# Kernel tuning notes

Hardware: AMD Instinct MI355X
Metric: run time of the kernel (lower is better)

The kernel has to match this reference:

```python
import jax, jax.numpy as jnp
import numpy as np

EPS = 1e-5

def _pw1d(W, b, x):  # W (O,C), x (B,C,N) -> (B,O,N); 1x1 Conv1d
    return jnp.einsum('oc,bcn->bon', W, x) + b[None, :, None]

def _pw2d(W, b, x):  # W (O,C), x (B,C,N,K) -> (B,O,N,K); 1x1 Conv2d
    return jnp.einsum('oc,bcnk->bonk', W, x) + b[None, :, None, None]

def _bn(x, g, b, m, v):  # BatchNorm2d, eval mode, over channel axis 1
    scale = g / jnp.sqrt(v + EPS)
    return (x - m[None, :, None, None]) * scale[None, :, None, None] + b[None, :, None, None]

def _knn(pos, k):  # pos (B,3,N) -> idx (B,N,K) of nearest neighbors (incl. self)
    p = jnp.transpose(pos, (0, 2, 1))             # (B,N,3)
    sq = jnp.sum(p * p, axis=-1)                  # (B,N)
    d = sq[:, :, None] - 2.0 * jnp.einsum('bid,bjd->bij', p, p) + sq[:, None, :]
    _, idx = jax.lax.top_k(-d, k)
    return idx

def _gather(feat, idx):  # feat (B,C,N), idx (B,N,K) -> (B,C,N,K)
    return jax.vmap(lambda f, i: f[:, i])(feat, idx)


def setup_inputs() -> dict:
    key = jax.random.key(0)
    B, C, N, H, AH, K = 4, 64, 4096, 64, 256, 16
    ks = jax.random.split(key, 32)
    s = lambda i, shp, sc=0.05: jax.random.normal(ks[i], shp, dtype=jnp.float32) * sc
    u = lambda i, shp: jax.random.uniform(ks[i], shp, dtype=jnp.float32, minval=0.5, maxval=1.5)
    return {
        'x': jax.random.normal(ks[0], (B, 3, N), dtype=jnp.float32),
        'y': jax.random.normal(ks[1], (B, C, N), dtype=jnp.float32),
        'W_start': s(2, (C, C)), 'b_start': s(3, (C,)),
        'W_key': s(4, (C, C)), 'b_key': s(5, (C,)),
        'W_query': s(6, (C, 3)), 'b_query': s(7, (C,)),
        'P1': s(8, (H, 3)), 'pb1': s(9, (H,)),
        'bn1_g': u(10, (H,)), 'bn1_b': s(11, (H,)), 'bn1_m': s(12, (H,)), 'bn1_v': u(13, (H,)),
        'P2': s(14, (C, H)), 'pb2': s(15, (C,)),
        'A1': s(16, (AH, C)), 'ab1': s(17, (AH,)),
        'bn2_g': u(18, (AH,)), 'bn2_b': s(19, (AH,)), 'bn2_m': s(20, (AH,)), 'bn2_v': u(21, (AH,)),
        'A2': s(22, (C, AH)), 'ab2': s(23, (C,)),
        'W_end': s(24, (C, C)), 'b_end': s(25, (C,)),
        'n_knn': 16,
    }


def reference(x, y, W_start, b_start, W_key, b_key, W_query, b_query,
              P1, pb1, bn1_g, bn1_b, bn1_m, bn1_v, P2, pb2,
              A1, ab1, bn2_g, bn2_b, bn2_m, bn2_v, A2, ab2,
              W_end, b_end, n_knn):
    identity = y
    y1 = _pw1d(W_start, b_start, y)                 # linear_start, (B,C,N)
    idx = _knn(x, n_knn)                            # (B,N,K)
    key = _pw1d(W_key, b_key, y1)
    value = y1
    query = _pw1d(W_query, b_query, x)              # 3 -> C pointwise
    key_g = _gather(key, idx)                       # (B,C,N,K)
    qk_rel = query[..., None] - key_g
    pos_rel = x[..., None] - _gather(x, idx)        # (B,3,N,K)
    pe = _pw2d(P2, pb2, jax.nn.relu(_bn(_pw2d(P1, pb1, pos_rel), bn1_g, bn1_b, bn1_m, bn1_v)))
    attn = _pw2d(A2, ab2, jax.nn.relu(_bn(_pw2d(A1, ab1, qk_rel + pe), bn2_g, bn2_b, bn2_m, bn2_v)))
    attn = jax.nn.softmax(attn, axis=-1)            # softmax over neighbor axis
    val = value[..., None] + pe                     # (B,C,N,K)
    agg = jnp.sum(attn * val, axis=-1)              # einsum 'bcij,bcij->bci'
    out = _pw1d(W_end, b_end, agg) + identity
    return out
```

## Files before the change

kernel.cpp:

```cpp
#include <hip/hip_runtime.h>
#include <hip/hip_bf16.h>

#define BB 4
#define CC 64
#define NN 4096
#define HH 64
#define AH 256
#define KNN 16
#define EPSV 1e-5f
#define PREP_NB 32

typedef __attribute__((ext_vector_type(8))) short short8;
typedef __attribute__((ext_vector_type(4))) short short4v;
typedef __attribute__((ext_vector_type(4))) unsigned short ushort4v;
typedef __attribute__((ext_vector_type(4))) float floatx4;

__device__ __forceinline__ unsigned short f2bf(float f) {
    unsigned u = __float_as_uint(f);
    u += 0x7FFFu + ((u >> 16) & 1u);
    return (unsigned short)(u >> 16);
}
__device__ __forceinline__ float bf2f(unsigned short u) {
    return __uint_as_float(((unsigned)u) << 16);
}

__device__ __forceinline__ unsigned long long umin64(unsigned long long a, unsigned long long b) {
    return a < b ? a : b;
}
__device__ __forceinline__ unsigned long long umax64(unsigned long long a, unsigned long long b) {
    return a > b ? a : b;
}
__device__ __forceinline__ unsigned long long shfl_xor_u64(unsigned long long v, int m) {
    int lo = __shfl_xor((int)(unsigned)(v & 0xFFFFFFFFull), m);
    int hi = __shfl_xor((int)(unsigned)(v >> 32), m);
    return ((unsigned long long)(unsigned)hi << 32) | (unsigned)lo;
}

__global__ void prep_params(const float* __restrict__ P1, const float* __restrict__ pb1,
                            const float* __restrict__ P2, const float* __restrict__ A1,
                            const float* __restrict__ ab1, const float* __restrict__ A2,
                            const float* __restrict__ g1, const float* __restrict__ b1,
                            const float* __restrict__ m1, const float* __restrict__ v1,
                            const float* __restrict__ g2, const float* __restrict__ b2,
                            const float* __restrict__ m2, const float* __restrict__ v2,
                            const float* __restrict__ Wend, const float* __restrict__ Ws,
                            const float* __restrict__ Wk, const float* __restrict__ Wq,
                            const float* __restrict__ bq,
                            unsigned short* __restrict__ A1L, unsigned short* __restrict__ A2L,
                            unsigned short* __restrict__ P2L, unsigned short* __restrict__ WendL,
                            unsigned short* __restrict__ WsL, unsigned short* __restrict__ WkL,
                            float* __restrict__ Wq4, float* __restrict__ P1p,
                            float* __restrict__ ab1f, float* __restrict__ bn2s_c) {
    int t0 = threadIdx.x;
    int t = blockIdx.x * 256 + t0;
    const int stride = PREP_NB * 256;
    if (blockIdx.x == 0) {
        if (t0 < HH) {
            float s = g1[t0] * rsqrtf(v1[t0] + EPSV);
            float c = b1[t0] - m1[t0] * s;
            P1p[4 * t0 + 0] = P1[3 * t0 + 0] * s;
            P1p[4 * t0 + 1] = P1[3 * t0 + 1] * s;
            P1p[4 * t0 + 2] = P1[3 * t0 + 2] * s;
            P1p[4 * t0 + 3] = pb1[t0] * s + c;
        }
        if (t0 < AH) {
            float s = g2[t0] * rsqrtf(v2[t0] + EPSV);
            bn2s_c[t0] = s;
            ab1f[t0] = ab1[t0] * s + (b2[t0] - m2[t0] * s);
        }
        if (t0 < CC) {
            Wq4[4 * t0 + 0] = Wq[3 * t0 + 0];
            Wq4[4 * t0 + 1] = Wq[3 * t0 + 1];
            Wq4[4 * t0 + 2] = Wq[3 * t0 + 2];
            Wq4[4 * t0 + 3] = bq[t0];
        }
    }
    for (int i = t; i < 16384; i += stride) {
        int e = i & 7, lane = (i >> 3) & 63, ks = (i >> 9) & 1, ht = i >> 10;
        int m = lane & 15, q = lane >> 4;
        A1L[i] = f2bf(A1[(ht * 16 + m) * CC + ks * 32 + q * 8 + e]);
    }
    for (int i = t; i < 16384; i += stride) {
        int e = i & 7, lane = (i >> 3) & 63, kk = (i >> 9) & 7, nt = i >> 12;
        int m = lane & 15, q = lane >> 4;
        A2L[i] = f2bf(A2[(nt * 16 + m) * AH + kk * 32 + q * 8 + e]);
    }
    for (int i = t; i < 4096; i += stride) {
        int e = i & 7, lane = (i >> 3) & 63, ks = (i >> 9) & 1, nt = i >> 10;
        int m = lane & 15, q = lane >> 4;
        P2L[i] = f2bf(P2[(nt * 16 + m) * HH + ks * 32 + q * 8 + e]);
    }
    for (int i = t; i < 4096; i += stride) {
        int e = i & 7, lane = (i >> 3) & 63, ks = (i >> 9) & 1, wv = i >> 10;
        int m = lane & 15, q = lane >> 4;
        WendL[i] = f2bf(Wend[(wv * 16 + m) * CC + ks * 32 + q * 8 + e]);
    }
    for (int i = t; i < 8192; i += stride) {
        int e = i & 7, lane = (i >> 3) & 63, ks = (i >> 9) & 1, ot = i >> 10;
        int m = lane & 15, q = lane >> 4;
        WsL[i] = f2bf(Ws[(ot * 16 + m) * CC + ks * 32 + q * 8 + e]);
    }
    for (int i = t; i < 8192; i += stride) {
        int e = i & 7, lane = (i >> 3) & 63, ks = (i >> 9) & 1, ot = i >> 10;
        int m = lane & 15, q = lane >> 4;
        WkL[i] = f2bf(Wk[(ot * 16 + m) * CC + ks * 32 + q * 8 + e]);
    }
}

#define UPITCH 68
#define HPITCH 68

__device__ __forceinline__ short8 lds_frag(const unsigned short* p) {
    short4v lo = *(const short4v*)p;
    short4v hi = *(const short4v*)(p + 4);
    short8 v;
    v[0] = lo[0]; v[1] = lo[1]; v[2] = lo[2]; v[3] = lo[3];
    v[4] = hi[0]; v[5] = hi[1]; v[6] = hi[2]; v[7] = hi[3];
    return v;
}

__global__ __launch_bounds__(64) void prep_features(
    const float* __restrict__ x, const float* __restrict__ y,
    const unsigned short* __restrict__ WsL, const float* __restrict__ bs,
    const unsigned short* __restrict__ WkL, const float* __restrict__ bk,
    const float* __restrict__ Wq4,
    unsigned short* __restrict__ y1bf, unsigned short* __restrict__ keybf,
    unsigned short* __restrict__ qrybf) {
    __shared__ unsigned short t_lds[16 * UPITCH];

    int b = blockIdx.x >> 8;
    int n0 = (blockIdx.x & 255) << 4;
    int lane = threadIdx.x;
    int m = lane & 15, quad = lane >> 4;
    size_t ybase = (size_t)b * CC * NN;

    short8 yA[2];
#pragma unroll
    for (int ks = 0; ks < 2; ++ks)
#pragma unroll
        for (int j = 0; j < 8; ++j)
            yA[ks][j] = (short)f2bf(y[ybase + (size_t)(ks * 32 + quad * 8 + j) * NN + n0 + m]);

#pragma unroll
    for (int ot = 0; ot < 4; ++ot) {
        short8 b0 = *(const short8*)(WsL + ((ot * 2 + 0) * 64 + lane) * 8);
        short8 b1 = *(const short8*)(WsL + ((ot * 2 + 1) * 64 + lane) * 8);
        floatx4 acc = (floatx4){0.f, 0.f, 0.f, 0.f};
        acc = __builtin_amdgcn_mfma_f32_16x16x32_bf16(yA[0], b0, acc, 0, 0, 0);
        acc = __builtin_amdgcn_mfma_f32_16x16x32_bf16(yA[1], b1, acc, 0, 0, 0);
        float bsv = bs[ot * 16 + m];
#pragma unroll
        for (int r = 0; r < 4; ++r)
            t_lds[(4 * quad + r) * UPITCH + ot * 16 + m] = f2bf(acc[r] + bsv);
    }
    __syncthreads();

    short8 uA[2];
#pragma unroll
    for (int ks = 0; ks < 2; ++ks)
        uA[ks] = lds_frag(&t_lds[m * UPITCH + ks * 32 + quad * 8]);

    int p = lane >> 2, ck = lane & 3;
    size_t obase = ((size_t)b * NN + n0 + p) * CC + ck * 16;
#pragma unroll
    for (int s = 0; s < 4; ++s)
        *(ushort4v*)(y1bf + obase + s * 4) =
            *(const ushort4v*)&t_lds[p * UPITCH + ck * 16 + s * 4];
    __syncthreads();

#pragma unroll
    for (int ot = 0; ot < 4; ++ot) {
        short8 b0 = *(const short8*)(WkL + ((ot * 2 + 0) * 64 + lane) * 8);
        short8 b1 = *(const short8*)(WkL + ((ot * 2 + 1) * 64 + lane) * 8);
        floatx4 acc = (floatx4){0.f, 0.f, 0.f, 0.f};
        acc = __builtin_amdgcn_mfma_f32_16x16x32_bf16(uA[0], b0, acc, 0, 0, 0);
        acc = __builtin_amdgcn_mfma_f32_16x16x32_bf16(uA[1], b1, acc, 0, 0, 0);
        float bkv = bk[ot * 16 + m];
#pragma unroll
        for (int r = 0; r < 4; ++r)
            t_lds[(4 * quad + r) * UPITCH + ot * 16 + m] = f2bf(acc[r] + bkv);
    }
    __syncthreads();
#pragma unroll
    for (int s = 0; s < 4; ++s)
        *(ushort4v*)(keybf + obase + s * 4) =
            *(const ushort4v*)&t_lds[p * UPITCH + ck * 16 + s * 4];

    float x0 = x[(size_t)(b * 3 + 0) * NN + n0 + p];
    float x1 = x[(size_t)(b * 3 + 1) * NN + n0 + p];
    float x2 = x[(size_t)(b * 3 + 2) * NN + n0 + p];
#pragma unroll
    for (int s = 0; s < 4; ++s) {
        ushort4v pk;
#pragma unroll
        for (int e = 0; e < 4; ++e) {
            int ch = ck * 16 + s * 4 + e;
            const float4 w = *(const float4*)(Wq4 + 4 * ch);
            pk[e] = f2bf(w.x * x0 + w.y * x1 + w.z * x2 + w.w);
        }
        *(ushort4v*)(qrybf + obase + s * 4) = pk;
    }
}

__global__ __launch_bounds__(256) void knn_kernel(const float* __restrict__ x,
                                                  int* __restrict__ idx_out) {
    __shared__ __align__(16) char smem[65536];
    float4* pts = (float4*)smem;
    unsigned long long* surv = (unsigned long long*)smem;

    int b = blockIdx.x >> 10;
    int grp = blockIdx.x & 1023;
    int w = threadIdx.x >> 6;
    int lane = threadIdx.x & 63;
    int n = (grp << 2) + w;

    const float* xb = x + (size_t)b * 3 * NN;
    for (int i = threadIdx.x; i < NN; i += 256)
        pts[i] = make_float4(xb[i], xb[NN + i], xb[2 * NN + i], 0.f);
    __syncthreads();

    float4 q = pts[n];

    float dreg[64];
    float vmin = 3.4e38f;
#pragma unroll
    for (int r = 0; r < 64; ++r) {
        float4 c = pts[(r << 6) + lane];
        float ax = q.x - c.x, ay = q.y - c.y, az = q.z - c.z;
        float d = ax * ax + ay * ay + az * az;
        dreg[r] = d;
        vmin = fminf(vmin, d);
    }
#pragma unroll
    for (int k = 2; k <= 64; k <<= 1) {
#pragma unroll
        for (int j = k >> 1; j > 0; j >>= 1) {
            float o = __shfl_xor(vmin, j);
            bool lower = (lane & j) == 0;
            bool up = (lane & k) == 0;
            float mn = fminf(vmin, o), mx = fmaxf(vmin, o);
            vmin = (lower == up) ? mn : mx;
        }
    }
    float T = __shfl(vmin, 15);

    __syncthreads();

    unsigned long long* buf = surv + (w << 7);
    unsigned cnt = 0;
#pragma unroll
    for (int r = 0; r < 64; ++r) {
        float d = dreg[r];
        bool hit = d <= T;
        unsigned long long mask = __ballot(hit);
        if (hit) {
            unsigned off = cnt + (unsigned)__popcll(mask & ((1ull << lane) - 1ull));
            if (off < 128) {
                int j = (r << 6) + lane;
                buf[off] = ((unsigned long long)__float_as_uint(d) << 32) | (unsigned)j;
            }
        }
        cnt += (unsigned)__popcll(mask);
    }
    if (cnt > 128) cnt = 128;

    unsigned long long v0 = (lane < (int)cnt) ? buf[lane] : 0xFFFFFFFFFFFFFFFFull;
    unsigned long long v1 = (lane + 64 < (int)cnt) ? buf[lane + 64] : 0xFFFFFFFFFFFFFFFFull;
#pragma unroll
    for (int k = 2; k <= 128; k <<= 1) {
#pragma unroll
        for (int j = k >> 1; j > 0; j >>= 1) {
            if (j >= 64) {
                unsigned long long lo = umin64(v0, v1), hi = umax64(v0, v1);
                v0 = lo; v1 = hi;
            } else {
                bool lower = (lane & j) == 0;
                unsigned long long o0 = shfl_xor_u64(v0, j);
                bool up0 = ((lane & k) == 0);
                v0 = (lower == up0) ? umin64(v0, o0) : umax64(v0, o0);
                unsigned long long o1 = shfl_xor_u64(v1, j);
                bool up1 = (((64 + lane) & k) == 0);
                v1 = (lower == up1) ? umin64(v1, o1) : umax64(v1, o1);
            }
        }
    }
    if (lane < KNN)
        idx_out[((size_t)b * NN + n) * KNN + lane] = (int)(unsigned)(v0 & 0xFFFFFFFFull);
}

__global__ __launch_bounds__(256, 3) void attn_mfma(
    const float* __restrict__ x, const float* __restrict__ y,
    const unsigned short* __restrict__ y1bf, const unsigned short* __restrict__ keybf,
    const unsigned short* __restrict__ qrybf, const int* __restrict__ idx,
    const float* __restrict__ P1p, const unsigned short* __restrict__ P2L,
    const float* __restrict__ pb2, const unsigned short* __restrict__ A1L,
    const float* __restrict__ ab1f, const float* __restrict__ bn2s_c,
    const unsigned short* __restrict__ A2L, const unsigned short* __restrict__ WendL,
    const float* __restrict__ bend,
    float* __restrict__ out) {
    __shared__ unsigned short u_lds[128 * UPITCH];
    __shared__ unsigned short hid_lds[128 * HPITCH];
    __shared__ float agg_lds[8 * 68];
    __shared__ float outstage[512];

    int blk = blockIdx.x;
    int b = blk & 3;
    int n0 = (blk >> 2) << 3;
    int w = threadIdx.x >> 6;
    int lane = threadIdx.x & 63;
    int m = lane & 15, quad = lane >> 4;

    int pt[2];
    size_t bpt[2];
#pragma unroll
    for (int t = 0; t < 2; ++t) {
        pt[t] = n0 + 2 * w + t;
        bpt[t] = (size_t)b * NN + pt[t];
    }

    int jm[2], j4[2][4];
    unsigned short qu[2][4], kvu[2][4][4];
#pragma unroll
    for (int t = 0; t < 2; ++t) {
        jm[t] = idx[bpt[t] * KNN + m];
#pragma unroll
        for (int r = 0; r < 4; ++r) j4[t][r] = idx[bpt[t] * KNN + 4 * quad + r];
#pragma unroll
        for (int nt = 0; nt < 4; ++nt) {
            qu[t][nt] = qrybf[bpt[t] * CC + nt * 16 + m];
#pragma unroll
            for (int r = 0; r < 4; ++r)
                kvu[t][nt][r] = keybf[((size_t)b * NN + j4[t][r]) * CC + nt * 16 + m];
        }
    }

    short8 h1A[2][2];
#pragma unroll
    for (int t = 0; t < 2; ++t) {
        float dx = x[(size_t)(b * 3 + 0) * NN + pt[t]] - x[(size_t)(b * 3 + 0) * NN + jm[t]];
        float dy = x[(size_t)(b * 3 + 1) * NN + pt[t]] - x[(size_t)(b * 3 + 1) * NN + jm[t]];
        float dz = x[(size_t)(b * 3 + 2) * NN + pt[t]] - x[(size_t)(b * 3 + 2) * NN + jm[t]];
#pragma unroll
        for (int ks = 0; ks < 2; ++ks)
#pragma unroll
            for (int j = 0; j < 8; ++j) {
                int h1 = ks * 32 + quad * 8 + j;
                const float4 p = *(const float4*)(P1p + 4 * h1);
                float a = fmaxf(p.x * dx + p.y * dy + p.z * dz + p.w, 0.f);
                h1A[t][ks][j] = (short)f2bf(a);
            }
    }

    floatx4 pacc[2][4];
#pragma unroll
    for (int t = 0; t < 2; ++t)
#pragma unroll
        for (int nt = 0; nt < 4; ++nt) pacc[t][nt] = (floatx4){0.f, 0.f, 0.f, 0.f};
#pragma unroll
    for (int ks = 0; ks < 2; ++ks)
#pragma unroll
        for (int nt = 0; nt < 4; ++nt) {
            short8 bb = *(const short8*)(P2L + ((nt * 2 + ks) * 64 + lane) * 8);
            pacc[0][nt] = __builtin_amdgcn_mfma_f32_16x16x32_bf16(h1A[0][ks], bb, pacc[0][nt], 0, 0, 0);
            pacc[1][nt] = __builtin_amdgcn_mfma_f32_16x16x32_bf16(h1A[1][ks], bb, pacc[1][nt], 0, 0, 0);
        }
#pragma unroll
    for (int nt = 0; nt < 4; ++nt) {
        float pb = pb2[nt * 16 + m];
#pragma unroll
        for (int t = 0; t < 2; ++t)
#pragma unroll
            for (int r = 0; r < 4; ++r) pacc[t][nt][r] += pb;
    }

#pragma unroll
    for (int t = 0; t < 2; ++t)
#pragma unroll
        for (int nt = 0; nt < 4; ++nt) {
            float qv = bf2f(qu[t][nt]);
#pragma unroll
            for (int r = 0; r < 4; ++r) {
                float uu = qv - bf2f(kvu[t][nt][r]) + pacc[t][nt][r];
                u_lds[(w * 32 + t * 16 + 4 * quad + r) * UPITCH + nt * 16 + m] = f2bf(uu);
            }
        }

    short8 uA[2][2];
#pragma unroll
    for (int t = 0; t < 2; ++t)
#pragma unroll
        for (int ks = 0; ks < 2; ++ks)
            uA[t][ks] = lds_frag(&u_lds[(w * 32 + t * 16 + m) * UPITCH + ks * 32 + quad * 8]);

    floatx4 acc2[2][4];
#pragma unroll
    for (int t = 0; t < 2; ++t)
#pragma unroll
        for (int nt = 0; nt < 4; ++nt) acc2[t][nt] = (floatx4){0.f, 0.f, 0.f, 0.f};

    for (int qd = 0; qd < 4; ++qd) {
#pragma unroll
        for (int nt4 = 0; nt4 < 4; ++nt4) {
            int ht = qd * 4 + nt4;
            const unsigned short* a1t = A1L + ht * 1024 + lane * 8;
            short8 b0 = *(const short8*)(a1t);
            short8 b1 = *(const short8*)(a1t + 512);
            int h = ht * 16 + m;
            float s = bn2s_c[h], t0 = ab1f[h];
#pragma unroll
            for (int t = 0; t < 2; ++t) {
                floatx4 acc = (floatx4){0.f, 0.f, 0.f, 0.f};
                acc = __builtin_amdgcn_mfma_f32_16x16x32_bf16(uA[t][0], b0, acc, 0, 0, 0);
                acc = __builtin_amdgcn_mfma_f32_16x16x32_bf16(uA[t][1], b1, acc, 0, 0, 0);
#pragma unroll
                for (int r = 0; r < 4; ++r) {
                    float hv = fmaxf(acc[r] * s + t0, 0.f);
                    hid_lds[(w * 32 + t * 16 + 4 * quad + r) * HPITCH + nt4 * 16 + m] = f2bf(hv);
                }
            }
        }
        short8 hA[2][2];
#pragma unroll
        for (int t = 0; t < 2; ++t)
#pragma unroll
            for (int ks = 0; ks < 2; ++ks)
                hA[t][ks] = lds_frag(&hid_lds[(w * 32 + t * 16 + m) * HPITCH + ks * 32 + quad * 8]);
#pragma unroll
        for (int ks = 0; ks < 2; ++ks)
#pragma unroll
            for (int nt = 0; nt < 4; ++nt) {
                int kk = qd * 2 + ks;
                short8 bb = *(const short8*)(A2L + ((nt * 8 + kk) * 64 + lane) * 8);
                acc2[0][nt] = __builtin_amdgcn_mfma_f32_16x16x32_bf16(hA[0][ks], bb, acc2[0][nt], 0, 0, 0);
                acc2[1][nt] = __builtin_amdgcn_mfma_f32_16x16x32_bf16(hA[1][ks], bb, acc2[1][nt], 0, 0, 0);
            }
    }

#pragma unroll
    for (int t = 0; t < 2; ++t)
#pragma unroll
        for (int nt = 0; nt < 4; ++nt) {
            float l0 = acc2[t][nt][0], l1 = acc2[t][nt][1];
            float l2 = acc2[t][nt][2], l3 = acc2[t][nt][3];
            float mx = fmaxf(fmaxf(l0, l1), fmaxf(l2, l3));
            mx = fmaxf(mx, __shfl_xor(mx, 16));
            mx = fmaxf(mx, __shfl_xor(mx, 32));
            float e0 = __expf(l0 - mx), e1 = __expf(l1 - mx);
            float e2 = __expf(l2 - mx), e3 = __expf(l3 - mx);
            float sum = (e0 + e1) + (e2 + e3);
            sum += __shfl_xor(sum, 16);
            sum += __shfl_xor(sum, 32);
            float y1v = bf2f(y1bf[bpt[t] * CC + nt * 16 + m]);
            float contrib = e0 * (y1v + pacc[t][nt][0]) + e1 * (y1v + pacc[t][nt][1]) +
                            e2 * (y1v + pacc[t][nt][2]) + e3 * (y1v + pacc[t][nt][3]);
            contrib += __shfl_xor(contrib, 16);
            contrib += __shfl_xor(contrib, 32);
            float agg = contrib / sum;
            if (quad == 0) agg_lds[(2 * w + t) * 68 + nt * 16 + m] = agg;
        }
    __syncthreads();

    short8 aggA[2];
#pragma unroll
    for (int ks = 0; ks < 2; ++ks)
#pragma unroll
        for (int j = 0; j < 8; ++j)
            aggA[ks][j] = (short)f2bf(agg_lds[(m & 7) * 68 + ks * 32 + quad * 8 + j]);
    short8 wb0 = *(const short8*)(WendL + ((w * 2 + 0) * 64 + lane) * 8);
    short8 wb1 = *(const short8*)(WendL + ((w * 2 + 1) * 64 + lane) * 8);
    floatx4 facc = (floatx4){0.f, 0.f, 0.f, 0.f};
    facc = __builtin_amdgcn_mfma_f32_16x16x32_bf16(aggA[0], wb0, facc, 0, 0, 0);
    facc = __builtin_amdgcn_mfma_f32_16x16x32_bf16(aggA[1], wb1, facc, 0, 0, 0);
    if (quad < 2) {
        float be = bend[w * 16 + m];
#pragma unroll
        for (int r = 0; r < 4; ++r)
            outstage[(w * 16 + m) * 8 + 4 * quad + r] = facc[r] + be;
    }
    __syncthreads();

    int t2 = threadIdx.x;
    int o = t2 >> 2, pp = (t2 & 3) * 2;
#pragma unroll
    for (int e = 0; e < 2; ++e) {
        size_t oi = ((size_t)(b * CC + o)) * NN + n0 + pp + e;
        out[oi] = outstage[o * 8 + pp + e] + y[oi];
    }
}

extern "C" void kernel_launch(void* const* d_in, const int* in_sizes, int n_in,
                              void* d_out, int out_size, void* d_ws, size_t ws_size,
                              hipStream_t stream) {
    const float* x    = (const float*)d_in[0];
    const float* y    = (const float*)d_in[1];
    const float* Ws   = (const float*)d_in[2];
    const float* bs   = (const float*)d_in[3];
    const float* Wk   = (const float*)d_in[4];
    const float* bk   = (const float*)d_in[5];
    const float* Wq   = (const float*)d_in[6];
    const float* bq   = (const float*)d_in[7];
    const float* P1   = (const float*)d_in[8];
    const float* pb1  = (const float*)d_in[9];
    const float* g1   = (const float*)d_in[10];
    const float* b1   = (const float*)d_in[11];
    const float* m1   = (const float*)d_in[12];
    const float* v1   = (const float*)d_in[13];
    const float* P2   = (const float*)d_in[14];
    const float* pb2  = (const float*)d_in[15];
    const float* A1   = (const float*)d_in[16];
    const float* ab1  = (const float*)d_in[17];
    const float* g2   = (const float*)d_in[18];
    const float* b2   = (const float*)d_in[19];
    const float* m2   = (const float*)d_in[20];
    const float* v2   = (const float*)d_in[21];
    const float* A2   = (const float*)d_in[22];
    const float* ab2  = (const float*)d_in[23];
    const float* Wend = (const float*)d_in[24];
    const float* bend = (const float*)d_in[25];
    (void)ab2;

    unsigned short* usws = (unsigned short*)d_ws;
    unsigned short* y1bf  = usws;
    unsigned short* keybf = usws + 1048576;
    unsigned short* qrybf = usws + 2097152;
    int* idx = (int*)(usws + 3145728);
    unsigned short* A1L = usws + 3670016;
    unsigned short* A2L = A1L + 16384;
    unsigned short* P2L = A2L + 16384;
    unsigned short* WsL = P2L + 4096;
    unsigned short* WkL = WsL + 8192;
    unsigned short* WendL = WkL + 8192;
    float* Wq4   = (float*)(WendL + 4096);
    float* P1p   = Wq4 + 256;
    float* ab1f  = P1p + 256;
    float* bn2sc = ab1f + 256;
    float* out   = (float*)d_out;

    hipLaunchKernelGGL(prep_params, dim3(PREP_NB), dim3(256), 0, stream,
                       P1, pb1, P2, A1, ab1, A2, g1, b1, m1, v1, g2, b2, m2, v2,
                       Wend, Ws, Wk, Wq, bq,
                       A1L, A2L, P2L, WendL, WsL, WkL, Wq4, P1p, ab1f, bn2sc);
    hipLaunchKernelGGL(prep_features, dim3(1024), dim3(64), 0, stream,
                       x, y, WsL, bs, WkL, bk, Wq4, y1bf, keybf, qrybf);
    hipLaunchKernelGGL(knn_kernel, dim3(4096), dim3(256), 0, stream, x, idx);
    hipLaunchKernelGGL(attn_mfma, dim3(2048), dim3(256), 0, stream,
                       x, y, y1bf, keybf, qrybf, idx,
                       P1p, P2L, pb2, A1L, ab1f, bn2sc, A2L, WendL,
                       bend, out);
}
```

Before: 242.0 us.

## Fuse param prep, feature prep and kNN into one heterogeneous kernel

Merges the three pre-attention kernels into a single launch whose blocks branch by index into kNN, feature projection, or parameter-relayout roles. This removes two launches and their serialization. The kNN path now handles two query points per wave, and the distance uses an expanded form with precomputed squared norms plus a monotone float-to-uint key. Feature blocks convert the Ws/Wk weights to bf16 on the fly instead of reading a prelaid buffer. Risks include register pressure from two 64-entry distance arrays, the 64KB LDS footprint now applying to the feature and param blocks too, and small numeric differences from the expanded distance formula.

```diff
diff --git a/kernel.cpp b/kernel.cpp
--- a/kernel.cpp
+++ b/kernel.cpp
@@ -8,7 +8,10 @@
 #define AH 256
 #define KNN 16
 #define EPSV 1e-5f
-#define PREP_NB 32
+
+#define KNN_BLKS 2048
+#define PF_BLKS 256
+#define PP_BLKS 32
 
 typedef __attribute__((ext_vector_type(8))) short short8;
 typedef __attribute__((ext_vector_type(4))) short short4v;
@@ -23,7 +26,6 @@
 __device__ __forceinline__ float bf2f(unsigned short u) {
     return __uint_as_float(((unsigned)u) << 16);
 }
-
 __device__ __forceinline__ unsigned long long umin64(unsigned long long a, unsigned long long b) {
     return a < b ? a : b;
 }
@@ -35,76 +37,9 @@
     int hi = __shfl_xor((int)(unsigned)(v >> 32), m);
     return ((unsigned long long)(unsigned)hi << 32) | (unsigned)lo;
 }
-
-__global__ void prep_params(const float* __restrict__ P1, const float* __restrict__ pb1,
-                            const float* __restrict__ P2, const float* __restrict__ A1,
-                            const float* __restrict__ ab1, const float* __restrict__ A2,
-                            const float* __restrict__ g1, const float* __restrict__ b1,
-                            const float* __restrict__ m1, const float* __restrict__ v1,
-                            const float* __restrict__ g2, const float* __restrict__ b2,
-                            const float* __restrict__ m2, const float* __restrict__ v2,
-                            const float* __restrict__ Wend, const float* __restrict__ Ws,
-                            const float* __restrict__ Wk, const float* __restrict__ Wq,
-                            const float* __restrict__ bq,
-                            unsigned short* __restrict__ A1L, unsigned short* __restrict__ A2L,
-                            unsigned short* __restrict__ P2L, unsigned short* __restrict__ WendL,
-                            unsigned short* __restrict__ WsL, unsigned short* __restrict__ WkL,
-                            float* __restrict__ Wq4, float* __restrict__ P1p,
-                            float* __restrict__ ab1f, float* __restrict__ bn2s_c) {
-    int t0 = threadIdx.x;
-    int t = blockIdx.x * 256 + t0;
-    const int stride = PREP_NB * 256;
-    if (blockIdx.x == 0) {
-        if (t0 < HH) {
-            float s = g1[t0] * rsqrtf(v1[t0] + EPSV);
-            float c = b1[t0] - m1[t0] * s;
-            P1p[4 * t0 + 0] = P1[3 * t0 + 0] * s;
-            P1p[4 * t0 + 1] = P1[3 * t0 + 1] * s;
-            P1p[4 * t0 + 2] = P1[3 * t0 + 2] * s;
-            P1p[4 * t0 + 3] = pb1[t0] * s + c;
-        }
-        if (t0 < AH) {
-            float s = g2[t0] * rsqrtf(v2[t0] + EPSV);
-            bn2s_c[t0] = s;
-            ab1f[t0] = ab1[t0] * s + (b2[t0] - m2[t0] * s);
-        }
-        if (t0 < CC) {
-            Wq4[4 * t0 + 0] = Wq[3 * t0 + 0];
-            Wq4[4 * t0 + 1] = Wq[3 * t0 + 1];
-            Wq4[4 * t0 + 2] = Wq[3 * t0 + 2];
-            Wq4[4 * t0 + 3] = bq[t0];
-        }
-    }
-    for (int i = t; i < 16384; i += stride) {
-        int e = i & 7, lane = (i >> 3) & 63, ks = (i >> 9) & 1, ht = i >> 10;
-        int m = lane & 15, q = lane >> 4;
-        A1L[i] = f2bf(A1[(ht * 16 + m) * CC + ks * 32 + q * 8 + e]);
-    }
-    for (int i = t; i < 16384; i += stride) {
-        int e = i & 7, lane = (i >> 3) & 63, kk = (i >> 9) & 7, nt = i >> 12;
-        int m = lane & 15, q = lane >> 4;
-        A2L[i] = f2bf(A2[(nt * 16 + m) * AH + kk * 32 + q * 8 + e]);
-    }
-    for (int i = t; i < 4096; i += stride) {
-        int e = i & 7, lane = (i >> 3) & 63, ks = (i >> 9) & 1, nt = i >> 10;
-        int m = lane & 15, q = lane >> 4;
-        P2L[i] = f2bf(P2[(nt * 16 + m) * HH + ks * 32 + q * 8 + e]);
-    }
-    for (int i = t; i < 4096; i += stride) {
-        int e = i & 7, lane = (i >> 3) & 63, ks = (i >> 9) & 1, wv = i >> 10;
-        int m = lane & 15, q = lane >> 4;
-        WendL[i] = f2bf(Wend[(wv * 16 + m) * CC + ks * 32 + q * 8 + e]);
-    }
-    for (int i = t; i < 8192; i += stride) {
-        int e = i & 7, lane = (i >> 3) & 63, ks = (i >> 9) & 1, ot = i >> 10;
-        int m = lane & 15, q = lane >> 4;
-        WsL[i] = f2bf(Ws[(ot * 16 + m) * CC + ks * 32 + q * 8 + e]);
-    }
-    for (int i = t; i < 8192; i += stride) {
-        int e = i & 7, lane = (i >> 3) & 63, ks = (i >> 9) & 1, ot = i >> 10;
-        int m = lane & 15, q = lane >> 4;
-        WkL[i] = f2bf(Wk[(ot * 16 + m) * CC + ks * 32 + q * 8 + e]);
-    }
+__device__ __forceinline__ unsigned fmono(float d) {
+    unsigned u = __float_as_uint(d);
+    return ((int)u < 0) ? ~u : (u | 0x80000000u);
 }
 
 #define UPITCH 68
@@ -119,173 +54,261 @@
     return v;
 }
 
-__global__ __launch_bounds__(64) void prep_features(
+__global__ __launch_bounds__(256) void fused_prep_knn(
     const float* __restrict__ x, const float* __restrict__ y,
-    const unsigned short* __restrict__ WsL, const float* __restrict__ bs,
-    const unsigned short* __restrict__ WkL, const float* __restrict__ bk,
-    const float* __restrict__ Wq4,
+    const float* __restrict__ Ws, const float* __restrict__ bs,
+    const float* __restrict__ Wk, const float* __restrict__ bk,
+    const float* __restrict__ Wq, const float* __restrict__ bq,
+    const float* __restrict__ P1, const float* __restrict__ pb1,
+    const float* __restrict__ P2, const float* __restrict__ A1,
+    const float* __restrict__ ab1, const float* __restrict__ A2,
+    const float* __restrict__ g1, const float* __restrict__ b1v,
+    const float* __restrict__ m1, const float* __restrict__ v1,
+    const float* __restrict__ g2, const float* __restrict__ b2v,
+    const float* __restrict__ m2, const float* __restrict__ v2,
+    const float* __restrict__ Wend,
+    int* __restrict__ idx_out,
     unsigned short* __restrict__ y1bf, unsigned short* __restrict__ keybf,
-    unsigned short* __restrict__ qrybf) {
-    __shared__ unsigned short t_lds[16 * UPITCH];
-
-    int b = blockIdx.x >> 8;
-    int n0 = (blockIdx.x & 255) << 4;
-    int lane = threadIdx.x;
-    int m = lane & 15, quad = lane >> 4;
-    size_t ybase = (size_t)b * CC * NN;
-
-    short8 yA[2];
-#pragma unroll
-    for (int ks = 0; ks < 2; ++ks)
-#pragma unroll
-        for (int j = 0; j < 8; ++j)
-            yA[ks][j] = (short)f2bf(y[ybase + (size_t)(ks * 32 + quad * 8 + j) * NN + n0 + m]);
-
-#pragma unroll
-    for (int ot = 0; ot < 4; ++ot) {
-        short8 b0 = *(const short8*)(WsL + ((ot * 2 + 0) * 64 + lane) * 8);
-        short8 b1 = *(const short8*)(WsL + ((ot * 2 + 1) * 64 + lane) * 8);
-        floatx4 acc = (floatx4){0.f, 0.f, 0.f, 0.f};
-        acc = __builtin_amdgcn_mfma_f32_16x16x32_bf16(yA[0], b0, acc, 0, 0, 0);
-        acc = __builtin_amdgcn_mfma_f32_16x16x32_bf16(yA[1], b1, acc, 0, 0, 0);
-        float bsv = bs[ot * 16 + m];
-#pragma unroll
-        for (int r = 0; r < 4; ++r)
-            t_lds[(4 * quad + r) * UPITCH + ot * 16 + m] = f2bf(acc[r] + bsv);
-    }
-    __syncthreads();
-
-    short8 uA[2];
-#pragma unroll
-    for (int ks = 0; ks < 2; ++ks)
-        uA[ks] = lds_frag(&t_lds[m * UPITCH + ks * 32 + quad * 8]);
-
-    int p = lane >> 2, ck = lane & 3;
-    size_t obase = ((size_t)b * NN + n0 + p) * CC + ck * 16;
-#pragma unroll
-    for (int s = 0; s < 4; ++s)
-        *(ushort4v*)(y1bf + obase + s * 4) =
-            *(const ushort4v*)&t_lds[p * UPITCH + ck * 16 + s * 4];
-    __syncthreads();
-
-#pragma unroll
-    for (int ot = 0; ot < 4; ++ot) {
-        short8 b0 = *(const short8*)(WkL + ((ot * 2 + 0) * 64 + lane) * 8);
-        short8 b1 = *(const short8*)(WkL + ((ot * 2 + 1) * 64 + lane) * 8);
-        floatx4 acc = (floatx4){0.f, 0.f, 0.f, 0.f};
-        acc = __builtin_amdgcn_mfma_f32_16x16x32_bf16(uA[0], b0, acc, 0, 0, 0);
-        acc = __builtin_amdgcn_mfma_f32_16x16x32_bf16(uA[1], b1, acc, 0, 0, 0);
-        float bkv = bk[ot * 16 + m];
-#pragma unroll
-        for (int r = 0; r < 4; ++r)
-            t_lds[(4 * quad + r) * UPITCH + ot * 16 + m] = f2bf(acc[r] + bkv);
-    }
-    __syncthreads();
-#pragma unroll
-    for (int s = 0; s < 4; ++s)
-        *(ushort4v*)(keybf + obase + s * 4) =
-            *(const ushort4v*)&t_lds[p * UPITCH + ck * 16 + s * 4];
-
-    float x0 = x[(size_t)(b * 3 + 0) * NN + n0 + p];
-    float x1 = x[(size_t)(b * 3 + 1) * NN + n0 + p];
-    float x2 = x[(size_t)(b * 3 + 2) * NN + n0 + p];
-#pragma unroll
-    for (int s = 0; s < 4; ++s) {
-        ushort4v pk;
-#pragma unroll
-        for (int e = 0; e < 4; ++e) {
-            int ch = ck * 16 + s * 4 + e;
-            const float4 w = *(const float4*)(Wq4 + 4 * ch);
-            pk[e] = f2bf(w.x * x0 + w.y * x1 + w.z * x2 + w.w);
-        }
-        *(ushort4v*)(qrybf + obase + s * 4) = pk;
-    }
-}
-
-__global__ __launch_bounds__(256) void knn_kernel(const float* __restrict__ x,
-                                                  int* __restrict__ idx_out) {
+    unsigned short* __restrict__ qrybf,
+    unsigned short* __restrict__ A1L, unsigned short* __restrict__ A2L,
+    unsigned short* __restrict__ P2L, unsigned short* __restrict__ WendL,
+    float* __restrict__ P1p, float* __restrict__ ab1f, float* __restrict__ bn2s_c) {
     __shared__ __align__(16) char smem[65536];
-    float4* pts = (float4*)smem;
-    unsigned long long* surv = (unsigned long long*)smem;
-
-    int b = blockIdx.x >> 10;
-    int grp = blockIdx.x & 1023;
+    int blk = blockIdx.x;
+    int lane = threadIdx.x & 63;
     int w = threadIdx.x >> 6;
-    int lane = threadIdx.x & 63;
-    int n = (grp << 2) + w;
-
-    const float* xb = x + (size_t)b * 3 * NN;
-    for (int i = threadIdx.x; i < NN; i += 256)
-        pts[i] = make_float4(xb[i], xb[NN + i], xb[2 * NN + i], 0.f);
-    __syncthreads();
-
-    float4 q = pts[n];
-
-    float dreg[64];
-    float vmin = 3.4e38f;
-#pragma unroll
-    for (int r = 0; r < 64; ++r) {
-        float4 c = pts[(r << 6) + lane];
-        float ax = q.x - c.x, ay = q.y - c.y, az = q.z - c.z;
-        float d = ax * ax + ay * ay + az * az;
-        dreg[r] = d;
-        vmin = fminf(vmin, d);
-    }
-#pragma unroll
-    for (int k = 2; k <= 64; k <<= 1) {
-#pragma unroll
-        for (int j = k >> 1; j > 0; j >>= 1) {
-            float o = __shfl_xor(vmin, j);
-            bool lower = (lane & j) == 0;
-            bool up = (lane & k) == 0;
-            float mn = fminf(vmin, o), mx = fmaxf(vmin, o);
-            vmin = (lower == up) ? mn : mx;
-        }
-    }
-    float T = __shfl(vmin, 15);
-
-    __syncthreads();
-
-    unsigned long long* buf = surv + (w << 7);
-    unsigned cnt = 0;
-#pragma unroll
-    for (int r = 0; r < 64; ++r) {
-        float d = dreg[r];
-        bool hit = d <= T;
-        unsigned long long mask = __ballot(hit);
-        if (hit) {
-            unsigned off = cnt + (unsigned)__popcll(mask & ((1ull << lane) - 1ull));
-            if (off < 128) {
-                int j = (r << 6) + lane;
-                buf[off] = ((unsigned long long)__float_as_uint(d) << 32) | (unsigned)j;
-            }
-        }
-        cnt += (unsigned)__popcll(mask);
-    }
-    if (cnt > 128) cnt = 128;
-
-    unsigned long long v0 = (lane < (int)cnt) ? buf[lane] : 0xFFFFFFFFFFFFFFFFull;
-    unsigned long long v1 = (lane + 64 < (int)cnt) ? buf[lane + 64] : 0xFFFFFFFFFFFFFFFFull;
-#pragma unroll
-    for (int k = 2; k <= 128; k <<= 1) {
-#pragma unroll
-        for (int j = k >> 1; j > 0; j >>= 1) {
-            if (j >= 64) {
-                unsigned long long lo = umin64(v0, v1), hi = umax64(v0, v1);
-                v0 = lo; v1 = hi;
-            } else {
-                bool lower = (lane & j) == 0;
-                unsigned long long o0 = shfl_xor_u64(v0, j);
-                bool up0 = ((lane & k) == 0);
-                v0 = (lower == up0) ? umin64(v0, o0) : umax64(v0, o0);
-                unsigned long long o1 = shfl_xor_u64(v1, j);
-                bool up1 = (((64 + lane) & k) == 0);
-                v1 = (lower == up1) ? umin64(v1, o1) : umax64(v1, o1);
-            }
-        }
-    }
-    if (lane < KNN)
-        idx_out[((size_t)b * NN + n) * KNN + lane] = (int)(unsigned)(v0 & 0xFFFFFFFFull);
+
+    if (blk < KNN_BLKS) {
+        float4* pts = (float4*)smem;
+        unsigned long long* surv = (unsigned long long*)smem;
+
+        int b = blk >> 9;
+        int grp = blk & 511;
+        const float* xb = x + (size_t)b * 3 * NN;
+        for (int i = threadIdx.x; i < NN; i += 256) {
+            float cx = xb[i], cy = xb[NN + i], cz = xb[2 * NN + i];
+            pts[i] = make_float4(cx, cy, cz, cx * cx + cy * cy + cz * cz);
+        }
+        __syncthreads();
+
+        int n0 = (grp << 3) + (w << 1);
+        float4 q0 = pts[n0], q1 = pts[n0 + 1];
+        float q0x = -2.f * q0.x, q0y = -2.f * q0.y, q0z = -2.f * q0.z, q0w = q0.w;
+        float q1x = -2.f * q1.x, q1y = -2.f * q1.y, q1z = -2.f * q1.z, q1w = q1.w;
+
+        float d0reg[64], d1reg[64];
+        float vmin0 = 3.4e38f, vmin1 = 3.4e38f;
+#pragma unroll
+        for (int r = 0; r < 64; ++r) {
+            float4 c = pts[(r << 6) + lane];
+            float d0 = fmaf(q0x, c.x, fmaf(q0y, c.y, fmaf(q0z, c.z, c.w + q0w)));
+            float d1 = fmaf(q1x, c.x, fmaf(q1y, c.y, fmaf(q1z, c.z, c.w + q1w)));
+            d0reg[r] = d0; d1reg[r] = d1;
+            vmin0 = fminf(vmin0, d0);
+            vmin1 = fminf(vmin1, d1);
+        }
+
+        float T[2];
+#pragma unroll
+        for (int t = 0; t < 2; ++t) {
+            float v = t ? vmin1 : vmin0;
+#pragma unroll
+            for (int k = 2; k <= 64; k <<= 1) {
+#pragma unroll
+                for (int j = k >> 1; j > 0; j >>= 1) {
+                    float o = __shfl_xor(v, j);
+                    bool lower = (lane & j) == 0;
+                    bool up = (lane & k) == 0;
+                    float mn = fminf(v, o), mx = fmaxf(v, o);
+                    v = (lower == up) ? mn : mx;
+                }
+            }
+            T[t] = __shfl(v, 15);
+        }
+        __syncthreads();
+
+#pragma unroll
+        for (int t = 0; t < 2; ++t) {
+            float Tt = T[t];
+            unsigned long long* buf = surv + (((w << 1) + t) << 7);
+            unsigned cnt = 0;
+#pragma unroll
+            for (int r = 0; r < 64; ++r) {
+                float d = t ? d1reg[r] : d0reg[r];
+                bool hit = d <= Tt;
+                unsigned long long mask = __ballot(hit);
+                if (hit) {
+                    unsigned off = cnt + (unsigned)__popcll(mask & ((1ull << lane) - 1ull));
+                    if (off < 128) {
+                        int j = (r << 6) + lane;
+                        buf[off] = ((unsigned long long)fmono(d) << 32) | (unsigned)j;
+                    }
+                }
+                cnt += (unsigned)__popcll(mask);
+            }
+            if (cnt > 128) cnt = 128;
+
+            unsigned long long v0 = (lane < (int)cnt) ? buf[lane] : 0xFFFFFFFFFFFFFFFFull;
+            unsigned long long v1 = (lane + 64 < (int)cnt) ? buf[lane + 64] : 0xFFFFFFFFFFFFFFFFull;
+#pragma unroll
+            for (int k = 2; k <= 128; k <<= 1) {
+#pragma unroll
+                for (int j = k >> 1; j > 0; j >>= 1) {
+                    if (j >= 64) {
+                        unsigned long long lo = umin64(v0, v1), hi = umax64(v0, v1);
+                        v0 = lo; v1 = hi;
+                    } else {
+                        bool lower = (lane & j) == 0;
+                        unsigned long long o0 = shfl_xor_u64(v0, j);
+                        bool up0 = ((lane & k) == 0);
+                        v0 = (lower == up0) ? umin64(v0, o0) : umax64(v0, o0);
+                        unsigned long long o1 = shfl_xor_u64(v1, j);
+                        bool up1 = (((64 + lane) & k) == 0);
+                        v1 = (lower == up1) ? umin64(v1, o1) : umax64(v1, o1);
+                    }
+                }
+            }
+            if (lane < KNN)
+                idx_out[((size_t)b * NN + n0 + t) * KNN + lane] =
+                    (int)(unsigned)(v0 & 0xFFFFFFFFull);
+        }
+    } else if (blk < KNN_BLKS + PF_BLKS) {
+        unsigned short* tl = (unsigned short*)smem + w * 16 * UPITCH;
+        int g4 = (blk - KNN_BLKS) * 4 + w;
+        int b = g4 >> 8;
+        int n0 = (g4 & 255) << 4;
+        int m = lane & 15, quad = lane >> 4;
+        size_t ybase = (size_t)b * CC * NN;
+
+        short8 yA[2];
+#pragma unroll
+        for (int ks = 0; ks < 2; ++ks)
+#pragma unroll
+            for (int j = 0; j < 8; ++j)
+                yA[ks][j] = (short)f2bf(y[ybase + (size_t)(ks * 32 + quad * 8 + j) * NN + n0 + m]);
+
+#pragma unroll
+        for (int ot = 0; ot < 4; ++ot) {
+            short8 bb0, bb1;
+#pragma unroll
+            for (int ks = 0; ks < 2; ++ks) {
+                const float* wr = Ws + (ot * 16 + m) * CC + ks * 32 + quad * 8;
+                float4 lo = *(const float4*)wr;
+                float4 hi = *(const float4*)(wr + 4);
+                short8 bb;
+                bb[0] = (short)f2bf(lo.x); bb[1] = (short)f2bf(lo.y);
+                bb[2] = (short)f2bf(lo.z); bb[3] = (short)f2bf(lo.w);
+                bb[4] = (short)f2bf(hi.x); bb[5] = (short)f2bf(hi.y);
+                bb[6] = (short)f2bf(hi.z); bb[7] = (short)f2bf(hi.w);
+                if (ks == 0) bb0 = bb; else bb1 = bb;
+            }
+            floatx4 acc = (floatx4){0.f, 0.f, 0.f, 0.f};
+            acc = __builtin_amdgcn_mfma_f32_16x16x32_bf16(yA[0], bb0, acc, 0, 0, 0);
+            acc = __builtin_amdgcn_mfma_f32_16x16x32_bf16(yA[1], bb1, acc, 0, 0, 0);
+            float bsv = bs[ot * 16 + m];
+#pragma unroll
+            for (int r = 0; r < 4; ++r)
+                tl[(4 * quad + r) * UPITCH + ot * 16 + m] = f2bf(acc[r] + bsv);
+        }
+        __syncthreads();
+
+        short8 uA[2];
+#pragma unroll
+        for (int ks = 0; ks < 2; ++ks)
+            uA[ks] = lds_frag(&tl[m * UPITCH + ks * 32 + quad * 8]);
+
+        int p = lane >> 2, ck = lane & 3;
+        size_t obase = ((size_t)b * NN + n0 + p) * CC + ck * 16;
+#pragma unroll
+        for (int s = 0; s < 4; ++s)
+            *(ushort4v*)(y1bf + obase + s * 4) =
+                *(const ushort4v*)&tl[p * UPITCH + ck * 16 + s * 4];
+        __syncthreads();
+
+#pragma unroll
+        for (int ot = 0; ot < 4; ++ot) {
+            short8 bb0, bb1;
+#pragma unroll
+            for (int ks = 0; ks < 2; ++ks) {
+                const float* wr = Wk + (ot * 16 + m) * CC + ks * 32 + quad * 8;
+                float4 lo = *(const float4*)wr;
+                float4 hi = *(const float4*)(wr + 4);
+                short8 bb;
+                bb[0] = (short)f2bf(lo.x); bb[1] = (short)f2bf(lo.y);
+                bb[2] = (short)f2bf(lo.z); bb[3] = (short)f2bf(lo.w);
+                bb[4] = (short)f2bf(hi.x); bb[5] = (short)f2bf(hi.y);
+                bb[6] = (short)f2bf(hi.z); bb[7] = (short)f2bf(hi.w);
+                if (ks == 0) bb0 = bb; else bb1 = bb;
+            }
+            floatx4 acc = (floatx4){0.f, 0.f, 0.f, 0.f};
+            acc = __builtin_amdgcn_mfma_f32_16x16x32_bf16(uA[0], bb0, acc, 0, 0, 0);
+            acc = __builtin_amdgcn_mfma_f32_16x16x32_bf16(uA[1], bb1, acc, 0, 0, 0);
+            float bkv = bk[ot * 16 + m];
+#pragma unroll
+            for (int r = 0; r < 4; ++r)
+                tl[(4 * quad + r) * UPITCH + ot * 16 + m] = f2bf(acc[r] + bkv);
+        }
+        __syncthreads();
+#pragma unroll
+        for (int s = 0; s < 4; ++s)
+            *(ushort4v*)(keybf + obase + s * 4) =
+                *(const ushort4v*)&tl[p * UPITCH + ck * 16 + s * 4];
+
+        float x0 = x[(size_t)(b * 3 + 0) * NN + n0 + p];
+        float x1 = x[(size_t)(b * 3 + 1) * NN + n0 + p];
+        float x2 = x[(size_t)(b * 3 + 2) * NN + n0 + p];
+#pragma unroll
+        for (int s = 0; s < 4; ++s) {
+            ushort4v pk;
+#pragma unroll
+            for (int e = 0; e < 4; ++e) {
+                int ch = ck * 16 + s * 4 + e;
+                pk[e] = f2bf(Wq[3 * ch + 0] * x0 + Wq[3 * ch + 1] * x1 +
+                             Wq[3 * ch + 2] * x2 + bq[ch]);
+            }
+            *(ushort4v*)(qrybf + obase + s * 4) = pk;
+        }
+    } else {
+        int pb = blk - KNN_BLKS - PF_BLKS;
+        int t0 = threadIdx.x;
+        int t = pb * 256 + t0;
+        const int stride = PP_BLKS * 256;
+        if (pb == 0) {
+            if (t0 < HH) {
+                float s = g1[t0] * rsqrtf(v1[t0] + EPSV);
+                float c = b1v[t0] - m1[t0] * s;
+                P1p[4 * t0 + 0] = P1[3 * t0 + 0] * s;
+                P1p[4 * t0 + 1] = P1[3 * t0 + 1] * s;
+                P1p[4 * t0 + 2] = P1[3 * t0 + 2] * s;
+                P1p[4 * t0 + 3] = pb1[t0] * s + c;
+            }
+            if (t0 < AH) {
+                float s = g2[t0] * rsqrtf(v2[t0] + EPSV);
+                bn2s_c[t0] = s;
+                ab1f[t0] = ab1[t0] * s + (b2v[t0] - m2[t0] * s);
+            }
+        }
+        for (int i = t; i < 16384; i += stride) {
+            int e = i & 7, ln = (i >> 3) & 63, ks = (i >> 9) & 1, ht = i >> 10;
+            int m = ln & 15, q = ln >> 4;
+            A1L[i] = f2bf(A1[(ht * 16 + m) * CC + ks * 32 + q * 8 + e]);
+        }
+        for (int i = t; i < 16384; i += stride) {
+            int e = i & 7, ln = (i >> 3) & 63, kk = (i >> 9) & 7, nt = i >> 12;
+            int m = ln & 15, q = ln >> 4;
+            A2L[i] = f2bf(A2[(nt * 16 + m) * AH + kk * 32 + q * 8 + e]);
+        }
+        for (int i = t; i < 4096; i += stride) {
+            int e = i & 7, ln = (i >> 3) & 63, ks = (i >> 9) & 1, nt = i >> 10;
+            int m = ln & 15, q = ln >> 4;
+            P2L[i] = f2bf(P2[(nt * 16 + m) * HH + ks * 32 + q * 8 + e]);
+        }
+        for (int i = t; i < 4096; i += stride) {
+            int e = i & 7, ln = (i >> 3) & 63, ks = (i >> 9) & 1, wv = i >> 10;
+            int m = ln & 15, q = ln >> 4;
+            WendL[i] = f2bf(Wend[(wv * 16 + m) * CC + ks * 32 + q * 8 + e]);
+        }
+    }
 }
 
 __global__ __launch_bounds__(256, 3) void attn_mfma(
@@ -527,22 +550,18 @@
     unsigned short* A1L = usws + 3670016;
     unsigned short* A2L = A1L + 16384;
     unsigned short* P2L = A2L + 16384;
-    unsigned short* WsL = P2L + 4096;
-    unsigned short* WkL = WsL + 8192;
-    unsigned short* WendL = WkL + 8192;
-    float* Wq4   = (float*)(WendL + 4096);
-    float* P1p   = Wq4 + 256;
+    unsigned short* WendL = P2L + 4096;
+    float* P1p   = (float*)(WendL + 4096);
     float* ab1f  = P1p + 256;
     float* bn2sc = ab1f + 256;
     float* out   = (float*)d_out;
 
-    hipLaunchKernelGGL(prep_params, dim3(PREP_NB), dim3(256), 0, stream,
-                       P1, pb1, P2, A1, ab1, A2, g1, b1, m1, v1, g2, b2, m2, v2,
-                       Wend, Ws, Wk, Wq, bq,
-                       A1L, A2L, P2L, WendL, WsL, WkL, Wq4, P1p, ab1f, bn2sc);
-    hipLaunchKernelGGL(prep_features, dim3(1024), dim3(64), 0, stream,
-                       x, y, WsL, bs, WkL, bk, Wq4, y1bf, keybf, qrybf);
-    hipLaunchKernelGGL(knn_kernel, dim3(4096), dim3(256), 0, stream, x, idx);
+    hipLaunchKernelGGL(fused_prep_knn, dim3(KNN_BLKS + PF_BLKS + PP_BLKS), dim3(256), 0, stream,
+                       x, y, Ws, bs, Wk, bk, Wq, bq,
+                       P1, pb1, P2, A1, ab1, A2,
+                       g1, b1, m1, v1, g2, b2, m2, v2, Wend,
+                       idx, y1bf, keybf, qrybf,
+                       A1L, A2L, P2L, WendL, P1p, ab1f, bn2sc);
     hipLaunchKernelGGL(attn_mfma, dim3(2048), dim3(256), 0, stream,
                        x, y, y1bf, keybf, qrybf, idx,
                        P1p, P2L, pb2, A1L, ab1f, bn2sc, A2L, WendL,
```

New measurement: 216.7 us. 10.4% less time.
